# Optimization experiments

Measured on AMD Instinct MI355X. Metric: run time of the kernel, lower is better.

## Reference

```python
import jax, jax.numpy as jnp
import numpy as np

E = 1024      # embed_dim
H = 16        # num_heads
HD = E // H   # head_dim = 64
WIN = 256     # window_size
LN_EPS = 1e-5


def _layernorm(x, g, b):
    mu = jnp.mean(x, axis=-1, keepdims=True)
    var = jnp.var(x, axis=-1, keepdims=True)
    return (x - mu) * jax.lax.rsqrt(var + LN_EPS) * g + b


def _rope_tables(S):
    freqs = 1.0 / (10000.0 ** (jnp.arange(0, HD, 2, dtype=jnp.float32) / HD))  # [HD/2]
    t = jnp.arange(S, dtype=jnp.float32)
    fr = jnp.outer(t, freqs)                      # [S, HD/2]
    emb = jnp.concatenate([fr, fr], axis=-1)      # [S, HD]
    # shape [S, 1, HD] so it broadcasts over the heads dim of [B, S, H, HD]
    return emb[:, None, :].astype(jnp.float32), None


def _rotate_half(x):
    x1, x2 = jnp.split(x, 2, axis=-1)
    return jnp.concatenate([-x2, x1], axis=-1)


def setup_inputs() -> dict:
    key = jax.random.key(0)
    ks = jax.random.split(key, 12)
    B, S = 8, 1024
    sc = 0.02
    return {
        "x": jax.random.normal(ks[0], (B, S, E), dtype=jnp.float32),
        "in_proj_w": jax.random.normal(ks[1], (3 * E, E), dtype=jnp.float32) * sc,
        "in_proj_b": jnp.zeros((3 * E,), dtype=jnp.float32),
        "out_proj_w": jax.random.normal(ks[2], (E, E), dtype=jnp.float32) * sc,
        "out_proj_b": jnp.zeros((E,), dtype=jnp.float32),
        "ln1_g": jnp.ones((E,), dtype=jnp.float32),
        "ln1_b": jnp.zeros((E,), dtype=jnp.float32),
        "w1": jax.random.normal(ks[3], (4 * E, E), dtype=jnp.float32) * sc,
        "b1": jnp.zeros((4 * E,), dtype=jnp.float32),
        "w2": jax.random.normal(ks[4], (E, 4 * E), dtype=jnp.float32) * sc,
        "b2": jnp.zeros((E,), dtype=jnp.float32),
        "ln2_g": jnp.ones((E,), dtype=jnp.float32),
        "ln2_b": jnp.zeros((E,), dtype=jnp.float32),
    }


def reference(x, in_proj_w, in_proj_b, out_proj_w, out_proj_b,
              ln1_g, ln1_b, w1, b1, w2, b2, ln2_g, ln2_b):
    B, S, _ = x.shape
    # RoPE applied to the raw input (pre in_proj), as in the torch module
    emb, _ = _rope_tables(S)
    cos, sin = jnp.cos(emb), jnp.sin(emb)          # [S, 1, HD]
    xh = x.reshape(B, S, H, HD)
    roped = xh * cos + _rotate_half(xh) * sin      # [B, S, H, HD]
    qk_in = roped.reshape(B, S, E)

    Wq, Wk, Wv = jnp.split(in_proj_w, 3, axis=0)   # each [E, E]
    bq, bk, bv = jnp.split(in_proj_b, 3, axis=0)
    q = (qk_in @ Wq.T + bq).reshape(B, S, H, HD).transpose(0, 2, 1, 3)  # [B,H,S,HD]
    k = (qk_in @ Wk.T + bk).reshape(B, S, H, HD).transpose(0, 2, 1, 3)
    v = (x @ Wv.T + bv).reshape(B, S, H, HD).transpose(0, 2, 1, 3)

    scale = 1.0 / np.sqrt(HD)
    scores = jnp.einsum("bhqd,bhkd->bhqk", q, k) * scale  # [B,H,S,S]
    idx = jnp.arange(S)
    disallowed = jnp.abs(idx[:, None] - idx[None, :]) > WIN  # [S,S] bool
    scores = jnp.where(disallowed, jnp.float32(-jnp.inf), scores)
    attn = jax.nn.softmax(scores, axis=-1)
    ctx = jnp.einsum("bhqk,bhkd->bhqd", attn, v)            # [B,H,S,HD]
    ctx = ctx.transpose(0, 2, 1, 3).reshape(B, S, E)
    h = ctx @ out_proj_w.T + out_proj_b

    x1 = _layernorm(x + h, ln1_g, ln1_b)
    ff = jax.nn.gelu(x1 @ w1.T + b1, approximate=False) @ w2.T + b2
    return _layernorm(x1 + ff, ln2_g, ln2_b)
```

## Files before the change

kernel.cpp:

```cpp
#include <hip/hip_runtime.h>
#include <stdint.h>


#define B_ 8
#define S_ 1024
#define E_ 1024
#define H_ 16
#define HD_ 64
#define WIN_ 256
#define QKV_ 3072

typedef __attribute__((ext_vector_type(8))) short short8;
typedef __attribute__((ext_vector_type(4))) float f32x4;
typedef __attribute__((ext_vector_type(4))) unsigned short us4;
typedef unsigned short ushort_t;

__device__ __forceinline__ ushort_t f2b(float f) {
  unsigned int u = __builtin_bit_cast(unsigned int, f);
  u = (u + 0x7fffu + ((u >> 16) & 1u)) >> 16;
  return (ushort_t)u;
}

__device__ __forceinline__ ushort_t f2b_trunc(float f) {
  return (ushort_t)(__builtin_bit_cast(unsigned int, f) >> 16);
}

__device__ __forceinline__ float fast_exp2(float x) {
#if __has_builtin(__builtin_amdgcn_exp2f)
  return __builtin_amdgcn_exp2f(x);
#else
  return exp2f(x);
#endif
}

__device__ __forceinline__ float fast_rcp(float x) {
#if __has_builtin(__builtin_amdgcn_rcpf)
  return __builtin_amdgcn_rcpf(x);
#else
  return 1.f / x;
#endif
}

__device__ __forceinline__ void gld_lds16(const void* g, void* l) {
  __builtin_amdgcn_global_load_lds((const __attribute__((address_space(1))) void*)g,
                                   (__attribute__((address_space(3))) void*)l, 16, 0, 0);
}

__global__ __launch_bounds__(256) void cast_bf16_kernel(const float* __restrict__ in,
                                                        ushort_t* __restrict__ out, int n4) {
  int i = blockIdx.x * 256 + threadIdx.x;
  if (i < n4) {
    float4 v = ((const float4*)in)[i];
    us4 o;
    o.x = f2b(v.x); o.y = f2b(v.y); o.z = f2b(v.z); o.w = f2b(v.w);
    ((us4*)out)[i] = o;
  }
}

__global__ __launch_bounds__(256) void rope_kernel(const float* __restrict__ x,
                                                   ushort_t* __restrict__ roped,
                                                   ushort_t* __restrict__ xbf) {
  int idx = blockIdx.x * 256 + threadIdx.x;
  int d = idx & 31;
  int h = (idx >> 5) & 15;
  int s = (idx >> 9) & 1023;
  int b = idx >> 19;
  size_t base = ((size_t)(b * S_ + s)) * E_ + h * HD_ + d;
  float x0 = x[base], x1 = x[base + 32];
  float freq = exp2f(-(float)d * 0.41524101186092029f);
  float th = (float)s * freq;
  float sn, cs;
  sincosf(th, &sn, &cs);
  roped[base]      = f2b(x0 * cs - x1 * sn);
  roped[base + 32] = f2b(x1 * cs + x0 * sn);
  xbf[base]      = f2b(x0);
  xbf[base + 32] = f2b(x1);
}

template <int MODE>
__global__ __launch_bounds__(256) void gemm_bt(const ushort_t* __restrict__ A,
                                               const ushort_t* __restrict__ A2,
                                               int nsplit,
                                               const ushort_t* __restrict__ Bm,
                                               const float* __restrict__ bias,
                                               void* __restrict__ C,
                                               int N, int K) {
  __shared__ ushort_t sA[128 * 32];
  __shared__ ushort_t sB[128 * 32];
  const int tid = threadIdx.x;
  const int lane = tid & 63;
  const int wave = tid >> 6;
  const int quad = lane >> 4;
  const int lq = lane & 15;
  const int wm = (wave & 1) * 64;
  const int wn = (wave >> 1) * 64;
  const size_t bm = (size_t)blockIdx.x * 128;
  const size_t bn = (size_t)blockIdx.y * 128;
  const ushort_t* Asel = (bn >= (size_t)nsplit) ? A2 : A;

  f32x4 acc[4][4] = {};

  const int srow = tid >> 2;
  const int skc = (((tid & 3) ^ ((tid >> 3) & 3)) * 8);
  const int csw = (quad ^ ((lq >> 1) & 3)) * 8;
  ushort_t* ldsA0 = &sA[wave * 512];
  ushort_t* ldsA1 = &sA[2048 + wave * 512];
  ushort_t* ldsB0 = &sB[wave * 512];
  ushort_t* ldsB1 = &sB[2048 + wave * 512];

  for (int k0 = 0; k0 < K; k0 += 32) {
    gld_lds16(Asel + (bm + srow) * K + k0 + skc, ldsA0);
    gld_lds16(Asel + (bm + 64 + srow) * K + k0 + skc, ldsA1);
    gld_lds16(Bm + (bn + srow) * K + k0 + skc, ldsB0);
    gld_lds16(Bm + (bn + 64 + srow) * K + k0 + skc, ldsB1);
    __syncthreads();

    short8 av[4], bv[4];
#pragma unroll
    for (int mt = 0; mt < 4; mt++)
      av[mt] = *(const short8*)&sA[(wm + mt * 16 + lq) * 32 + csw];
#pragma unroll
    for (int nt = 0; nt < 4; nt++)
      bv[nt] = *(const short8*)&sB[(wn + nt * 16 + lq) * 32 + csw];
#pragma unroll
    for (int mt = 0; mt < 4; mt++)
#pragma unroll
      for (int nt = 0; nt < 4; nt++)
        acc[mt][nt] = __builtin_amdgcn_mfma_f32_16x16x32_bf16(av[mt], bv[nt], acc[mt][nt], 0, 0, 0);
    __syncthreads();
  }

#pragma unroll
  for (int mt = 0; mt < 4; mt++) {
#pragma unroll
    for (int nt = 0; nt < 4; nt++) {
      size_t row = bm + wm + mt * 16 + quad * 4;
      size_t col = bn + wn + nt * 16 + lq;
      float bc = bias[col];
#pragma unroll
      for (int r = 0; r < 4; r++) {
        float v = acc[mt][nt][r] + bc;
        if (MODE == 1) {
          float y = 0.7978845608028654f * (v + 0.044715f * v * v * v);
          float t = fast_exp2(y * 2.8853900817779268f);
          v = v * (t * fast_rcp(1.f + t));
        }
        if (MODE == 2)
          ((float*)C)[(row + r) * N + col] = v;
        else
          ((ushort_t*)C)[(row + r) * N + col] = f2b(v);
      }
    }
  }
}

__global__ __launch_bounds__(256) void vtrans_kernel(const ushort_t* __restrict__ qkv,
                                                     ushort_t* __restrict__ vt) {
  __shared__ ushort_t tb[64 * 65];
  int bh = blockIdx.x >> 4;
  int st = blockIdx.x & 15;
  int b = bh >> 4, h = bh & 15;
  int s0 = st * 64;
  int tid = threadIdx.x;
  int c = tid & 63, rbase = tid >> 6;
#pragma unroll
  for (int rep = 0; rep < 16; rep++) {
    int i = rep * 4 + rbase;
    tb[c * 65 + i] = qkv[(size_t)(b * S_ + s0 + i) * QKV_ + 2048 + h * HD_ + c];
  }
  __syncthreads();
#pragma unroll
  for (int rep = 0; rep < 16; rep++) {
    int d = rep * 4 + rbase;
    vt[(size_t)((b * H_ + h) * HD_ + d) * S_ + s0 + c] = tb[d * 65 + c];
  }
}

#define SC_ 0.18033688011112042f

__global__ __launch_bounds__(256) void attn_kernel(const ushort_t* __restrict__ qkv,
                                                   const ushort_t* __restrict__ vt,
                                                   ushort_t* __restrict__ ctx) {
  __shared__ ushort_t sK[2][32 * 64];
  __shared__ ushort_t sV[2][64 * 32];
  __shared__ ushort_t sP[4][16 * 36];
  const int tid = threadIdx.x;
  const int lane = tid & 63, wave = tid >> 6;
  const int quad = lane >> 4, lq = lane & 15;
  int gid = ((blockIdx.x & 7) << 8) | (blockIdx.x >> 3);
  int qs = gid & 15;
  int h = (gid >> 4) & 15;
  int b = gid >> 8;
  int qs64 = qs * 64;
  int q0 = qs64 + wave * 16;

  const size_t qoff = (size_t)(b * S_ + q0 + lq) * QKV_ + h * HD_;
  short8 a0 = *(const short8*)&qkv[qoff + quad * 8];
  short8 a1 = *(const short8*)&qkv[qoff + 32 + quad * 8];

  f32x4 o[4] = {};
  float rs[4] = {0.f, 0.f, 0.f, 0.f};

  int start = qs64 - WIN_; if (start < 0) start = 0;
  int end = qs64 + 64 + WIN_; if (end > S_) end = S_;
  const int wlo = q0 - WIN_;
  const int whi = q0 + 16 + WIN_;

  const ushort_t* kg = qkv + (size_t)(b * S_) * QKV_ + 1024 + h * HD_;
  const ushort_t* vg = vt + (size_t)((b * H_ + h) * HD_) * S_;

  const int krow = lane >> 3;
  const int kchg = ((lane & 7) ^ krow) << 3;
  const int vrow = lane >> 2;
  const int vchg = ((lane & 3) ^ ((lane >> 3) & 3)) << 3;

  gld_lds16(kg + (size_t)(start + wave * 8 + krow) * QKV_ + kchg, &sK[0][wave * 512]);
  gld_lds16(vg + (size_t)(wave * 16 + vrow) * S_ + start + vchg, &sV[0][wave * 512]);

  const int nch = (end - start) >> 5;
  int buf = 0;
  for (int c = 0; c < nch; c++) {
    __syncthreads();
    int kb = start + c * 32;
    if (c + 1 < nch) {
      int nkb = kb + 32;
      gld_lds16(kg + (size_t)(nkb + wave * 8 + krow) * QKV_ + kchg, &sK[buf ^ 1][wave * 512]);
      gld_lds16(vg + (size_t)(wave * 16 + vrow) * S_ + nkb + vchg, &sV[buf ^ 1][wave * 512]);
    }
    if (kb < whi && kb + 32 > wlo) {
      f32x4 s[2];
#pragma unroll
      for (int t = 0; t < 2; t++) {
        const ushort_t* kr = &sK[buf][(t * 16 + lq) * 64];
        short8 b0 = *(const short8*)&kr[((quad ^ (lq & 7)) << 3)];
        short8 b1 = *(const short8*)&kr[(((4 + quad) ^ (lq & 7)) << 3)];
        f32x4 z = {};
        z = __builtin_amdgcn_mfma_f32_16x16x32_bf16(a0, b0, z, 0, 0, 0);
        z = __builtin_amdgcn_mfma_f32_16x16x32_bf16(a1, b1, z, 0, 0, 0);
        s[t] = z;
      }
      float p[2][4];
      const bool full = (kb >= q0 - 241) && (kb <= q0 + 225);
      if (full) {
#pragma unroll
        for (int t = 0; t < 2; t++)
#pragma unroll
          for (int r = 0; r < 4; r++) p[t][r] = fast_exp2(s[t][r] * SC_);
      } else {
#pragma unroll
        for (int t = 0; t < 2; t++) {
          int ki = kb + t * 16 + lq;
#pragma unroll
          for (int r = 0; r < 4; r++) {
            int dd = q0 + quad * 4 + r - ki;
            bool allowed = (dd <= WIN_) && (dd >= -WIN_);
            p[t][r] = allowed ? fast_exp2(s[t][r] * SC_) : 0.f;
          }
        }
      }
#pragma unroll
      for (int r = 0; r < 4; r++) rs[r] += p[0][r] + p[1][r];

#pragma unroll
      for (int t = 0; t < 2; t++)
#pragma unroll
        for (int r = 0; r < 4; r++)
          sP[wave][(quad * 4 + r) * 36 + t * 16 + lq] = f2b_trunc(p[t][r]);
      asm volatile("s_waitcnt lgkmcnt(0)" ::: "memory");
      short8 ap = *(const short8*)&sP[wave][lq * 36 + quad * 8];

#pragma unroll
      for (int nt = 0; nt < 4; nt++) {
        short8 bvf = *(const short8*)&sV[buf][(nt * 16 + lq) * 32 +
                                             ((quad ^ ((lq >> 1) & 3)) << 3)];
        o[nt] = __builtin_amdgcn_mfma_f32_16x16x32_bf16(ap, bvf, o[nt], 0, 0, 0);
      }
    }
    buf ^= 1;
  }

  float inv[4];
#pragma unroll
  for (int r = 0; r < 4; r++) {
    float v = rs[r];
    v += __shfl_xor(v, 1);
    v += __shfl_xor(v, 2);
    v += __shfl_xor(v, 4);
    v += __shfl_xor(v, 8);
    inv[r] = 1.f / v;
  }

#pragma unroll
  for (int nt = 0; nt < 4; nt++)
#pragma unroll
    for (int r = 0; r < 4; r++) {
      int row = q0 + quad * 4 + r;
      int col = h * HD_ + nt * 16 + lq;
      ctx[(size_t)(b * S_ + row) * E_ + col] = f2b(o[nt][r] * inv[r]);
    }
}

__global__ __launch_bounds__(256) void ln_res_kernel(const float* __restrict__ A,
                                                     const float* __restrict__ Bv,
                                                     const float* __restrict__ g,
                                                     const float* __restrict__ be,
                                                     float* __restrict__ outf,
                                                     ushort_t* __restrict__ outb) {
  const int row = blockIdx.x;
  const int tid = threadIdx.x;
  const size_t base = (size_t)row * 1024;
  float v[4];
  float s = 0.f, sq = 0.f;
#pragma unroll
  for (int i = 0; i < 4; i++) {
    int idx = i * 256 + tid;
    float y = A[base + idx] + Bv[base + idx];
    v[i] = y;
    s += y;
    sq += y * y;
  }
#pragma unroll
  for (int off = 32; off; off >>= 1) {
    s += __shfl_xor(s, off);
    sq += __shfl_xor(sq, off);
  }
  __shared__ float ls[4], lsq[4];
  int wave = tid >> 6, lane = tid & 63;
  if (lane == 0) { ls[wave] = s; lsq[wave] = sq; }
  __syncthreads();
  s = ls[0] + ls[1] + ls[2] + ls[3];
  sq = lsq[0] + lsq[1] + lsq[2] + lsq[3];
  float mean = s * (1.f / 1024.f);
  float var = sq * (1.f / 1024.f) - mean * mean;
  float rstd = rsqrtf(var + 1e-5f);
#pragma unroll
  for (int i = 0; i < 4; i++) {
    int idx = i * 256 + tid;
    float o = (v[i] - mean) * rstd * g[idx] + be[idx];
    outf[base + idx] = o;
    if (outb) outb[base + idx] = f2b(o);
  }
}

#define O_XBF   ((size_t)0)
#define O_ROPED ((size_t)16777216)
#define O_W_IN  ((size_t)33554432)
#define O_W_OUT ((size_t)39845888)
#define O_W1    ((size_t)41943040)
#define O_W2    ((size_t)50331648)
#define O_BIG   ((size_t)58720256)
#define O_VT    ((size_t)125829120)
#define O_X1F   ((size_t)142606336)
#define O_FF2   ((size_t)176160768)

extern "C" void kernel_launch(void* const* d_in, const int* in_sizes, int n_in,
                              void* d_out, int out_size, void* d_ws, size_t ws_size,
                              hipStream_t stream) {
  const float* x          = (const float*)d_in[0];
  const float* in_proj_w  = (const float*)d_in[1];
  const float* in_proj_b  = (const float*)d_in[2];
  const float* out_proj_w = (const float*)d_in[3];
  const float* out_proj_b = (const float*)d_in[4];
  const float* ln1_g      = (const float*)d_in[5];
  const float* ln1_b      = (const float*)d_in[6];
  const float* w1         = (const float*)d_in[7];
  const float* b1         = (const float*)d_in[8];
  const float* w2         = (const float*)d_in[9];
  const float* b2         = (const float*)d_in[10];
  const float* ln2_g      = (const float*)d_in[11];
  const float* ln2_b      = (const float*)d_in[12];
  float* out = (float*)d_out;

  char* ws = (char*)d_ws;
  ushort_t* xbf     = (ushort_t*)(ws + O_XBF);
  ushort_t* roped   = (ushort_t*)(ws + O_ROPED);
  ushort_t* wbf_in  = (ushort_t*)(ws + O_W_IN);
  ushort_t* wbf_out = (ushort_t*)(ws + O_W_OUT);
  ushort_t* wbf_1   = (ushort_t*)(ws + O_W1);
  ushort_t* wbf_2   = (ushort_t*)(ws + O_W2);
  ushort_t* qkv_buf = (ushort_t*)(ws + O_BIG);
  ushort_t* vtb     = (ushort_t*)(ws + O_VT);
  ushort_t* ctx     = (ushort_t*)(ws + O_ROPED);
  float*    h_f32   = (float*)(ws + O_BIG);
  float*    x1f     = (float*)(ws + O_X1F);
  ushort_t* x1bf    = (ushort_t*)(ws + O_XBF);
  ushort_t* ff1     = (ushort_t*)(ws + O_BIG);
  float*    ff2     = (float*)(ws + O_FF2);

  dim3 blk(256);
  const int NOSPLIT = 1 << 30;

  cast_bf16_kernel<<<dim3(3072), blk, 0, stream>>>(in_proj_w, wbf_in, 3145728 / 4);
  cast_bf16_kernel<<<dim3(1024), blk, 0, stream>>>(out_proj_w, wbf_out, 1048576 / 4);
  cast_bf16_kernel<<<dim3(4096), blk, 0, stream>>>(w1, wbf_1, 4194304 / 4);
  cast_bf16_kernel<<<dim3(4096), blk, 0, stream>>>(w2, wbf_2, 4194304 / 4);

  rope_kernel<<<dim3(16384), blk, 0, stream>>>(x, roped, xbf);

  gemm_bt<0><<<dim3(64, 24), blk, 0, stream>>>(roped, xbf, 2048, wbf_in, in_proj_b,
                                               qkv_buf, QKV_, 1024);
  vtrans_kernel<<<dim3(2048), blk, 0, stream>>>(qkv_buf, vtb);

  attn_kernel<<<dim3(2048), blk, 0, stream>>>(qkv_buf, vtb, ctx);

  gemm_bt<2><<<dim3(64, 8), blk, 0, stream>>>(ctx, ctx, NOSPLIT, wbf_out, out_proj_b,
                                              h_f32, 1024, 1024);

  ln_res_kernel<<<dim3(8192), blk, 0, stream>>>(x, h_f32, ln1_g, ln1_b, x1f, x1bf);

  gemm_bt<1><<<dim3(64, 32), blk, 0, stream>>>(x1bf, x1bf, NOSPLIT, wbf_1, b1,
                                               ff1, 4096, 1024);

  gemm_bt<2><<<dim3(64, 8), blk, 0, stream>>>(ff1, ff1, NOSPLIT, wbf_2, b2,
                                              ff2, 1024, 4096);

  ln_res_kernel<<<dim3(8192), blk, 0, stream>>>(x1f, ff2, ln2_g, ln2_b, out, nullptr);
}
```

Baseline: 514.6 us.

## Double GEMM K-tile, store projection outputs in bf16, merge weight casts, vectorize LayerNorm

The GEMM now stages a 64-wide K slice per iteration with a new XOR swizzle, which halves the number of barrier pairs per K loop. The out-proj and FFN2 GEMMs write bf16 instead of fp32, so the residual LayerNorm reads half the bytes; LayerNorm itself is rewritten with float4 and 4-wide loads. The four weight-cast launches are merged into one kernel. The bf16 intermediates add rounding error before the residual add.

```diff
diff --git a/kernel.cpp b/kernel.cpp
--- a/kernel.cpp
+++ b/kernel.cpp
@@ -25,6 +25,10 @@
   return (ushort_t)(__builtin_bit_cast(unsigned int, f) >> 16);
 }
 
+__device__ __forceinline__ float b2f(ushort_t u) {
+  return __builtin_bit_cast(float, ((unsigned int)u) << 16);
+}
+
 __device__ __forceinline__ float fast_exp2(float x) {
 #if __has_builtin(__builtin_amdgcn_exp2f)
   return __builtin_amdgcn_exp2f(x);
@@ -46,15 +50,26 @@
                                    (__attribute__((address_space(3))) void*)l, 16, 0, 0);
 }
 
-__global__ __launch_bounds__(256) void cast_bf16_kernel(const float* __restrict__ in,
-                                                        ushort_t* __restrict__ out, int n4) {
+__global__ __launch_bounds__(256) void cast4_kernel(const float* __restrict__ i0,
+                                                    const float* __restrict__ i1,
+                                                    const float* __restrict__ i2,
+                                                    const float* __restrict__ i3,
+                                                    ushort_t* __restrict__ o0,
+                                                    ushort_t* __restrict__ o1,
+                                                    ushort_t* __restrict__ o2,
+                                                    ushort_t* __restrict__ o3) {
   int i = blockIdx.x * 256 + threadIdx.x;
-  if (i < n4) {
-    float4 v = ((const float4*)in)[i];
-    us4 o;
-    o.x = f2b(v.x); o.y = f2b(v.y); o.z = f2b(v.z); o.w = f2b(v.w);
-    ((us4*)out)[i] = o;
-  }
+  const float* in;
+  ushort_t* out;
+  int j;
+  if (i < 786432)       { in = i0; out = o0; j = i; }
+  else if (i < 1048576) { in = i1; out = o1; j = i - 786432; }
+  else if (i < 2097152) { in = i2; out = o2; j = i - 1048576; }
+  else                  { in = i3; out = o3; j = i - 2097152; }
+  float4 v = ((const float4*)in)[j];
+  us4 o;
+  o.x = f2b(v.x); o.y = f2b(v.y); o.z = f2b(v.z); o.w = f2b(v.w);
+  ((us4*)out)[j] = o;
 }
 
 __global__ __launch_bounds__(256) void rope_kernel(const float* __restrict__ x,
@@ -83,10 +98,10 @@
                                                int nsplit,
                                                const ushort_t* __restrict__ Bm,
                                                const float* __restrict__ bias,
-                                               void* __restrict__ C,
+                                               ushort_t* __restrict__ C,
                                                int N, int K) {
-  __shared__ ushort_t sA[128 * 32];
-  __shared__ ushort_t sB[128 * 32];
+  __shared__ ushort_t sA[128 * 64];
+  __shared__ ushort_t sB[128 * 64];
   const int tid = threadIdx.x;
   const int lane = tid & 63;
   const int wave = tid >> 6;
@@ -100,33 +115,34 @@
 
   f32x4 acc[4][4] = {};
 
-  const int srow = tid >> 2;
-  const int skc = (((tid & 3) ^ ((tid >> 3) & 3)) * 8);
-  const int csw = (quad ^ ((lq >> 1) & 3)) * 8;
-  ushort_t* ldsA0 = &sA[wave * 512];
-  ushort_t* ldsA1 = &sA[2048 + wave * 512];
-  ushort_t* ldsB0 = &sB[wave * 512];
-  ushort_t* ldsB1 = &sB[2048 + wave * 512];
-
-  for (int k0 = 0; k0 < K; k0 += 32) {
-    gld_lds16(Asel + (bm + srow) * K + k0 + skc, ldsA0);
-    gld_lds16(Asel + (bm + 64 + srow) * K + k0 + skc, ldsA1);
-    gld_lds16(Bm + (bn + srow) * K + k0 + skc, ldsB0);
-    gld_lds16(Bm + (bn + 64 + srow) * K + k0 + skc, ldsB1);
+  const int srow = lane >> 3;
+  const int skc = ((lane & 7) ^ (lane >> 3)) * 8;
+
+  for (int k0 = 0; k0 < K; k0 += 64) {
+#pragma unroll
+    for (int i = 0; i < 4; i++) {
+      const int r0 = wave * 32 + i * 8;
+      gld_lds16(Asel + (bm + r0 + srow) * K + k0 + skc, &sA[r0 * 64]);
+      gld_lds16(Bm + (bn + r0 + srow) * K + k0 + skc, &sB[r0 * 64]);
+    }
     __syncthreads();
 
-    short8 av[4], bv[4];
-#pragma unroll
-    for (int mt = 0; mt < 4; mt++)
-      av[mt] = *(const short8*)&sA[(wm + mt * 16 + lq) * 32 + csw];
-#pragma unroll
-    for (int nt = 0; nt < 4; nt++)
-      bv[nt] = *(const short8*)&sB[(wn + nt * 16 + lq) * 32 + csw];
-#pragma unroll
-    for (int mt = 0; mt < 4; mt++)
+#pragma unroll
+    for (int kk = 0; kk < 2; kk++) {
+      const int csw = (((kk * 4) + quad) ^ (lq & 7)) * 8;
+      short8 av[4], bv[4];
+#pragma unroll
+      for (int mt = 0; mt < 4; mt++)
+        av[mt] = *(const short8*)&sA[(wm + mt * 16 + lq) * 64 + csw];
 #pragma unroll
       for (int nt = 0; nt < 4; nt++)
-        acc[mt][nt] = __builtin_amdgcn_mfma_f32_16x16x32_bf16(av[mt], bv[nt], acc[mt][nt], 0, 0, 0);
+        bv[nt] = *(const short8*)&sB[(wn + nt * 16 + lq) * 64 + csw];
+#pragma unroll
+      for (int mt = 0; mt < 4; mt++)
+#pragma unroll
+        for (int nt = 0; nt < 4; nt++)
+          acc[mt][nt] = __builtin_amdgcn_mfma_f32_16x16x32_bf16(av[mt], bv[nt], acc[mt][nt], 0, 0, 0);
+    }
     __syncthreads();
   }
 
@@ -145,10 +161,7 @@
           float t = fast_exp2(y * 2.8853900817779268f);
           v = v * (t * fast_rcp(1.f + t));
         }
-        if (MODE == 2)
-          ((float*)C)[(row + r) * N + col] = v;
-        else
-          ((ushort_t*)C)[(row + r) * N + col] = f2b(v);
+        C[(row + r) * N + col] = f2b(v);
       }
     }
   }
@@ -301,7 +314,7 @@
 }
 
 __global__ __launch_bounds__(256) void ln_res_kernel(const float* __restrict__ A,
-                                                     const float* __restrict__ Bv,
+                                                     const ushort_t* __restrict__ Bv,
                                                      const float* __restrict__ g,
                                                      const float* __restrict__ be,
                                                      float* __restrict__ outf,
@@ -309,16 +322,15 @@
   const int row = blockIdx.x;
   const int tid = threadIdx.x;
   const size_t base = (size_t)row * 1024;
+  float4 a4 = ((const float4*)(A + base))[tid];
+  us4 b4 = ((const us4*)(Bv + base))[tid];
   float v[4];
-  float s = 0.f, sq = 0.f;
-#pragma unroll
-  for (int i = 0; i < 4; i++) {
-    int idx = i * 256 + tid;
-    float y = A[base + idx] + Bv[base + idx];
-    v[i] = y;
-    s += y;
-    sq += y * y;
-  }
+  v[0] = a4.x + b2f(b4.x);
+  v[1] = a4.y + b2f(b4.y);
+  v[2] = a4.z + b2f(b4.z);
+  v[3] = a4.w + b2f(b4.w);
+  float s = v[0] + v[1] + v[2] + v[3];
+  float sq = v[0] * v[0] + v[1] * v[1] + v[2] * v[2] + v[3] * v[3];
 #pragma unroll
   for (int off = 32; off; off >>= 1) {
     s += __shfl_xor(s, off);
@@ -333,12 +345,18 @@
   float mean = s * (1.f / 1024.f);
   float var = sq * (1.f / 1024.f) - mean * mean;
   float rstd = rsqrtf(var + 1e-5f);
-#pragma unroll
-  for (int i = 0; i < 4; i++) {
-    int idx = i * 256 + tid;
-    float o = (v[i] - mean) * rstd * g[idx] + be[idx];
-    outf[base + idx] = o;
-    if (outb) outb[base + idx] = f2b(o);
+  float4 g4 = ((const float4*)g)[tid];
+  float4 e4 = ((const float4*)be)[tid];
+  float o0 = (v[0] - mean) * rstd * g4.x + e4.x;
+  float o1 = (v[1] - mean) * rstd * g4.y + e4.y;
+  float o2 = (v[2] - mean) * rstd * g4.z + e4.z;
+  float o3 = (v[3] - mean) * rstd * g4.w + e4.w;
+  float4 of = {o0, o1, o2, o3};
+  ((float4*)(outf + base))[tid] = of;
+  if (outb) {
+    us4 ob;
+    ob.x = f2b(o0); ob.y = f2b(o1); ob.z = f2b(o2); ob.w = f2b(o3);
+    ((us4*)(outb + base))[tid] = ob;
   }
 }
 
@@ -381,19 +399,17 @@
   ushort_t* qkv_buf = (ushort_t*)(ws + O_BIG);
   ushort_t* vtb     = (ushort_t*)(ws + O_VT);
   ushort_t* ctx     = (ushort_t*)(ws + O_ROPED);
-  float*    h_f32   = (float*)(ws + O_BIG);
+  ushort_t* h_bf    = (ushort_t*)(ws + O_BIG);
   float*    x1f     = (float*)(ws + O_X1F);
   ushort_t* x1bf    = (ushort_t*)(ws + O_XBF);
   ushort_t* ff1     = (ushort_t*)(ws + O_BIG);
-  float*    ff2     = (float*)(ws + O_FF2);
+  ushort_t* ff2     = (ushort_t*)(ws + O_FF2);
 
   dim3 blk(256);
   const int NOSPLIT = 1 << 30;
 
-  cast_bf16_kernel<<<dim3(3072), blk, 0, stream>>>(in_proj_w, wbf_in, 3145728 / 4);
-  cast_bf16_kernel<<<dim3(1024), blk, 0, stream>>>(out_proj_w, wbf_out, 1048576 / 4);
-  cast_bf16_kernel<<<dim3(4096), blk, 0, stream>>>(w1, wbf_1, 4194304 / 4);
-  cast_bf16_kernel<<<dim3(4096), blk, 0, stream>>>(w2, wbf_2, 4194304 / 4);
+  cast4_kernel<<<dim3(12288), blk, 0, stream>>>(in_proj_w, out_proj_w, w1, w2,
+                                                wbf_in, wbf_out, wbf_1, wbf_2);
 
   rope_kernel<<<dim3(16384), blk, 0, stream>>>(x, roped, xbf);
 
@@ -403,15 +419,15 @@
 
   attn_kernel<<<dim3(2048), blk, 0, stream>>>(qkv_buf, vtb, ctx);
 
-  gemm_bt<2><<<dim3(64, 8), blk, 0, stream>>>(ctx, ctx, NOSPLIT, wbf_out, out_proj_b,
-                                              h_f32, 1024, 1024);
-
-  ln_res_kernel<<<dim3(8192), blk, 0, stream>>>(x, h_f32, ln1_g, ln1_b, x1f, x1bf);
+  gemm_bt<0><<<dim3(64, 8), blk, 0, stream>>>(ctx, ctx, NOSPLIT, wbf_out, out_proj_b,
+                                              h_bf, 1024, 1024);
+
+  ln_res_kernel<<<dim3(8192), blk, 0, stream>>>(x, h_bf, ln1_g, ln1_b, x1f, x1bf);
 
   gemm_bt<1><<<dim3(64, 32), blk, 0, stream>>>(x1bf, x1bf, NOSPLIT, wbf_1, b1,
                                                ff1, 4096, 1024);
 
-  gemm_bt<2><<<dim3(64, 8), blk, 0, stream>>>(ff1, ff1, NOSPLIT, wbf_2, b2,
+  gemm_bt<0><<<dim3(64, 8), blk, 0, stream>>>(ff1, ff1, NOSPLIT, wbf_2, b2,
                                               ff2, 1024, 4096);
 
   ln_res_kernel<<<dim3(8192), blk, 0, stream>>>(x1f, ff2, ln2_g, ln2_b, out, nullptr);
```

Result: faster. 473.6 us (-8.0%).
